# Kernel optimization log

Hardware: AMD Instinct MI355X
Metric: run time of the kernel (lower is better)

Reference implementation:

```python
import jax, jax.numpy as jnp
import numpy as np

KH = KW = 3
K = KH * KW
PAD = 1


def conv3x3(x, w, b):
    # x: [B,C,H,W], w: [O,C,3,3], b: [O]
    y = jax.lax.conv_general_dilated(x, w, (1, 1), ((PAD, PAD), (PAD, PAD)),
                                     dimension_numbers=('NCHW', 'OIHW', 'NCHW'))
    return y + b[None, :, None, None]


def deform_conv(x, offsets, w, b):
    # torchvision DeformConv2d, stride=1, pad=1, dilation=1, groups=1, offset_groups=1
    # x: [B,C,H,W], offsets: [B,2*K,H,W] ordered (dy,dx) per kernel point, w: [O,C,3,3]
    B, C, H, W = x.shape
    O = w.shape[0]
    off = offsets.reshape(B, K, 2, H, W)
    dy, dx = off[:, :, 0], off[:, :, 1]                      # [B,K,H,W]
    kyy, kxx = jnp.meshgrid(jnp.arange(KH), jnp.arange(KW), indexing='ij')
    ky = kyy.reshape(K).astype(x.dtype)
    kx = kxx.reshape(K).astype(x.dtype)
    py = dy + ky[None, :, None, None] + jnp.arange(H, dtype=x.dtype)[None, None, :, None] - PAD
    px = dx + kx[None, :, None, None] + jnp.arange(W, dtype=x.dtype)[None, None, None, :] - PAD
    y0 = jnp.floor(py)
    x0 = jnp.floor(px)
    wy = (py - y0)[:, None]                                   # [B,1,K,H,W]
    wx = (px - x0)[:, None]
    y0i = y0.astype(jnp.int32)
    x0i = x0.astype(jnp.int32)
    xf = x.reshape(B, C, H * W)

    def gather(yi, xi):
        valid = (yi >= 0) & (yi < H) & (xi >= 0) & (xi < W)   # zero outside
        yc = jnp.clip(yi, 0, H - 1)
        xc = jnp.clip(xi, 0, W - 1)
        idx = (yc * W + xc).reshape(B, 1, K * H * W)
        g = jnp.take_along_axis(xf, idx, axis=2).reshape(B, C, K, H, W)
        return g * valid[:, None].astype(x.dtype)

    v00 = gather(y0i, x0i)
    v01 = gather(y0i, x0i + 1)
    v10 = gather(y0i + 1, x0i)
    v11 = gather(y0i + 1, x0i + 1)
    samp = (v00 * (1 - wy) * (1 - wx) + v01 * (1 - wy) * wx
            + v10 * wy * (1 - wx) + v11 * wy * wx)            # [B,C,K,H,W]
    out = jnp.einsum('bckhw,ock->bohw', samp, w.reshape(O, C, K))
    return out + b[None, :, None, None]


def deform_align(x, y, wo, bo, wd, bd):
    return deform_conv(x, conv3x3(y, wo, bo), wd, bd)


def setup_inputs() -> dict:
    key = jax.random.key(0)
    ks = jax.random.split(key, 16)
    inC, embedC = 64, 96
    B, H, W = 4, 96, 96
    s = 0.02
    d = {
        'x1': jax.random.normal(ks[0], (B, inC, H, W), jnp.float32),
        'y': jax.random.normal(ks[1], (B, inC, H, W), jnp.float32),
        # block 1: offset conv inC->2K, deform conv inC->embedC
        'wo1': jax.random.normal(ks[2], (2 * K, inC, 3, 3), jnp.float32) * s,
        'bo1': jnp.zeros((2 * K,), jnp.float32),
        'wd1': jax.random.normal(ks[3], (embedC, inC, 3, 3), jnp.float32) * s,
        'bd1': jnp.zeros((embedC,), jnp.float32),
        # block 2: embedC->2K, embedC->embedC
        'wo2': jax.random.normal(ks[4], (2 * K, embedC, 3, 3), jnp.float32) * s,
        'bo2': jnp.zeros((2 * K,), jnp.float32),
        'wd2': jax.random.normal(ks[5], (embedC, embedC, 3, 3), jnp.float32) * s,
        'bd2': jnp.zeros((embedC,), jnp.float32),
        # block 3: embedC->2K, embedC->inC
        'wo3': jax.random.normal(ks[6], (2 * K, embedC, 3, 3), jnp.float32) * s,
        'bo3': jnp.zeros((2 * K,), jnp.float32),
        'wd3': jax.random.normal(ks[7], (inC, embedC, 3, 3), jnp.float32) * s,
        'bd3': jnp.zeros((inC,), jnp.float32),
    }
    return d


def reference(x1, y, wo1, bo1, wd1, bd1, wo2, bo2, wd2, bd2, wo3, bo3, wd3, bd3):
    h = deform_align(x1, y, wo1, bo1, wd1, bd1)
    h = deform_align(h, h, wo2, bo2, wd2, bd2)
    h = deform_align(h, h, wo3, bo3, wd3, bd3)
    return h
```

## Files before the change

kernel.cpp:

```cpp
#include <hip/hip_runtime.h>

constexpr int B = 4, H = 96, W = 96, HW = H * W;
constexpr int NPIX = B * HW;
constexpr int KOFF = 18;

typedef _Float16 half8 __attribute__((ext_vector_type(8)));
typedef _Float16 half4 __attribute__((ext_vector_type(4)));
typedef float f32x4 __attribute__((ext_vector_type(4)));
typedef __attribute__((address_space(3))) _Float16 lf16;

__device__ __forceinline__ int iclamp(int v, int lo, int hi) {
  return v < lo ? lo : (v > hi ? hi : v);
}

struct Corners {
  int i00, i01, i10, i11;
  float w00, w01, w10, w11;
};

__device__ __forceinline__ Corners mk_corners(float py, float qx) {
  float fy = floorf(py), fx = floorf(qx);
  float wy = py - fy, wx = qx - fx;
  int y0 = (int)fy, x0 = (int)fx;
  int y1 = y0 + 1, x1 = x0 + 1;
  bool vy0 = (y0 >= 0) & (y0 < H);
  bool vy1 = (y1 >= 0) & (y1 < H);
  bool vx0 = (x0 >= 0) & (x0 < W);
  bool vx1 = (x1 >= 0) & (x1 < W);
  int r0 = iclamp(y0, 0, H - 1) * W;
  int r1 = iclamp(y1, 0, H - 1) * W;
  int c0 = iclamp(x0, 0, W - 1);
  int c1 = iclamp(x1, 0, W - 1);
  Corners cc;
  cc.i00 = r0 + c0; cc.i01 = r0 + c1; cc.i10 = r1 + c0; cc.i11 = r1 + c1;
  float a = 1.f - wy, bb = 1.f - wx;
  cc.w00 = a * bb * ((vy0 & vx0) ? 1.f : 0.f);
  cc.w01 = a * wx * ((vy0 & vx1) ? 1.f : 0.f);
  cc.w10 = wy * bb * ((vy1 & vx0) ? 1.f : 0.f);
  cc.w11 = wy * wx * ((vy1 & vx1) ? 1.f : 0.f);
  return cc;
}

__device__ __forceinline__ void vm_wait0() {
  asm volatile("s_waitcnt vmcnt(0)" ::: "memory");
  __builtin_amdgcn_sched_barrier(0);
}

__device__ __forceinline__ void gld_lds16(const _Float16* g, lf16* l) {
  __builtin_amdgcn_global_load_lds(
      (const __attribute__((address_space(1))) void*)g,
      (__attribute__((address_space(3))) void*)l, 16, 0, 0);
}

template <int NF>
__device__ __forceinline__ void stage_frags(const _Float16* wk, lf16* lb, int lane) {
#pragma unroll
  for (int f = 0; f < NF; ++f)
    gld_lds16(wk + (size_t)f * 512 + lane * 8, lb + f * 512);
}

template <int KS>
__device__ __forceinline__ void load_corners(const _Float16* xb, int ch, const Corners& cc,
                                             half8 r[KS][4]) {
  const _Float16* p00 = xb + (size_t)cc.i00 * (KS * 32) + ch;
  const _Float16* p01 = xb + (size_t)cc.i01 * (KS * 32) + ch;
  const _Float16* p10 = xb + (size_t)cc.i10 * (KS * 32) + ch;
  const _Float16* p11 = xb + (size_t)cc.i11 * (KS * 32) + ch;
#pragma unroll
  for (int ks = 0; ks < KS; ++ks) {
    r[ks][0] = *(const half8*)(p00 + ks * 32);
    r[ks][1] = *(const half8*)(p01 + ks * 32);
    r[ks][2] = *(const half8*)(p10 + ks * 32);
    r[ks][3] = *(const half8*)(p11 + ks * 32);
  }
}

template <int KS>
__device__ __forceinline__ void interp_corners(const Corners& cc, half8 r[KS][4],
                                               half8 a[KS]) {
  _Float16 q00 = (_Float16)cc.w00, q01 = (_Float16)cc.w01;
  _Float16 q10 = (_Float16)cc.w10, q11 = (_Float16)cc.w11;
#pragma unroll
  for (int ks = 0; ks < KS; ++ks)
    a[ks] = r[ks][0] * q00 + r[ks][1] * q01 + r[ks][2] * q10 + r[ks][3] * q11;
}

template <int KS>
__device__ __forceinline__ void load_shift(const _Float16* xb, int ch, int h, int w,
                                           int ky, int kx, half8 a[KS]) {
  int yy = h + ky, xx = w + kx;
  bool v = (yy >= 0) & (yy < H) & (xx >= 0) & (xx < W);
  int yc = iclamp(yy, 0, H - 1), xc = iclamp(xx, 0, W - 1);
  const _Float16* pv = xb + (size_t)(yc * W + xc) * (KS * 32) + ch;
#pragma unroll
  for (int ks = 0; ks < KS; ++ks) {
    half8 r = *(const half8*)(pv + ks * 32);
    half8 z = {0, 0, 0, 0, 0, 0, 0, 0};
    a[ks] = v ? r : z;
  }
}

template <int KS, int NJ>
__device__ __forceinline__ void mfma_lds(const _Float16* lb, int lane,
                                         half8 a[KS], f32x4 acc[NJ]) {
#pragma unroll
  for (int ks = 0; ks < KS; ++ks)
#pragma unroll
    for (int j = 0; j < NJ; ++j) {
      half8 b = *(const half8*)(lb + (ks * NJ + j) * 512 + lane * 8);
      acc[j] = __builtin_amdgcn_mfma_f32_16x16x32_f16(a[ks], b, acc[j], 0, 0, 0);
    }
}

struct WAll {
  const float* src[6];
  _Float16* dst[6];
  int C[6], Osrc[6], OPAD[6], base[6];
};

__global__ void wfrag_all_kernel(WAll wa) {
  int bid = blockIdx.x;
  int s = 0;
#pragma unroll
  for (int i = 1; i < 6; ++i) s += (bid >= wa.base[i]) ? 1 : 0;
  int fid = bid - wa.base[s];
  int C = wa.C[s], Osrc = wa.Osrc[s], OPAD = wa.OPAD[s];
  const float* wsrc = wa.src[s];
  _Float16* wf = wa.dst[s];
  int KS = C / 32;
  int NJ = OPAD / 16;
  int lane = threadIdx.x;
  int j = fid % NJ;
  int ks = (fid / NJ) % KS;
  int k = fid / (NJ * KS);
  int o = j * 16 + (lane & 15);
  int c0 = ks * 32 + (lane >> 4) * 8;
  half8 v;
#pragma unroll
  for (int u = 0; u < 8; ++u)
    v[u] = (o < Osrc) ? (_Float16)wsrc[((size_t)o * C + c0 + u) * 9 + k] : (_Float16)0.f;
  *(half8*)(wf + ((size_t)fid * 64 + lane) * 8) = v;
}

__global__ __launch_bounds__(256) void repack2_kernel(const float* __restrict__ in0,
                                                      const float* __restrict__ in1,
                                                      _Float16* __restrict__ o0,
                                                      _Float16* __restrict__ o1) {
  constexpr int C = 64;
  const float* in = blockIdx.y ? in1 : in0;
  _Float16* outh = blockIdx.y ? o1 : o0;
  __shared__ float tile[64 * C];
  int t = threadIdx.x;
  int pix0 = blockIdx.x * 64;
  int b = pix0 / HW;
  int hw0 = pix0 - b * HW;
  int l = t & 63;
  for (int cc = t >> 6; cc < C; cc += 4)
    tile[cc * 64 + l] = in[((size_t)b * C + cc) * HW + hw0 + l];
  __syncthreads();
  int pl = t >> 2;
  int cq = t & 3;
  _Float16* op = outh + (size_t)(pix0 + pl) * C + cq * (C / 4);
#pragma unroll
  for (int c = 0; c < C / 4; c += 4) {
    half4 hv;
#pragma unroll
    for (int u = 0; u < 4; ++u) hv[u] = (_Float16)tile[(cq * (C / 4) + c + u) * 64 + pl];
    *(half4*)(op + c) = hv;
  }
}

template <int C, int O, bool WF32, bool WH>
__global__ __launch_bounds__(64, 1)
void stage_kernel(const _Float16* __restrict__ xoff, const _Float16* __restrict__ xdef,
                  const _Float16* __restrict__ wfo, const float* __restrict__ bo,
                  const _Float16* __restrict__ wfd, const float* __restrict__ bd,
                  float* __restrict__ out, _Float16* __restrict__ outh) {
  constexpr int KS = C / 32;
  constexpr int NJ = O / 16;
  constexpr int NFD = KS * NJ;
  constexpr int NFO = KS * 2;
  __shared__ _Float16 ldsB[2 * NFD * 512];
  __shared__ float lofs[16][KOFF];
  lf16* lb3 = (lf16*)ldsB;
  const int lane = threadIdx.x;
  const int row = lane & 15;
  const int kgrp = lane >> 4;
  const int ch = kgrp * 8;
  const int chunk = (blockIdx.x & 7) * (int)(gridDim.x >> 3) + (blockIdx.x >> 3);
  const int px0 = chunk * 16;
  const int b = px0 / HW;
  const int hw0 = px0 - b * HW;
  const int hwm = hw0 + row;
  const int h0 = hwm / W, w0 = hwm - h0 * W;
  const _Float16* xo = xoff + (size_t)b * HW * C;
  const _Float16* xd = xdef + (size_t)b * HW * C;

  {
    f32x4 aoc[2];
#pragma unroll
    for (int j = 0; j < 2; ++j) {
      int o = j * 16 + row;
      float bv = (o < KOFF) ? bo[o] : 0.f;
      aoc[j] = {bv, bv, bv, bv};
    }
    half8 a[KS], n[KS];
    stage_frags<NFO>(wfo, lb3, lane);
    load_shift<KS>(xo, ch, h0, w0, -1, -1, a);
#pragma unroll
    for (int k = 0; k < 9; ++k) {
      vm_wait0();
      if (k < 8) {
        int kn = k + 1;
        stage_frags<NFO>(wfo + (size_t)kn * (NFO * 512),
                         lb3 + (kn & 1) * NFO * 512, lane);
        load_shift<KS>(xo, ch, h0, w0, kn / 3 - 1, kn % 3 - 1, n);
        __builtin_amdgcn_sched_barrier(0);
      }
      mfma_lds<KS, 2>(ldsB + (k & 1) * NFO * 512, lane, a, aoc);
      if (k < 8) {
#pragma unroll
        for (int ks = 0; ks < KS; ++ks) a[ks] = n[ks];
      }
    }
#pragma unroll
    for (int j = 0; j < 2; ++j) {
      int o = j * 16 + row;
      if (o < KOFF) {
#pragma unroll
        for (int r = 0; r < 4; ++r) lofs[kgrp * 4 + r][o] = aoc[j][r];
      }
    }
  }

  const float hf = (float)(h0 - 1), wwf = (float)(w0 - 1);

  f32x4 acc[NJ];
#pragma unroll
  for (int j = 0; j < NJ; ++j) {
    float bv = bd[j * 16 + row];
    acc[j] = {bv, bv, bv, bv};
  }
  half8 a[KS];
  half8 r[KS][4], rn[KS][4];
  Corners ccur = mk_corners(lofs[row][0] + hf, lofs[row][1] + wwf);
  stage_frags<NFD>(wfd, lb3 + NFD * 512, lane);
  load_corners<KS>(xd, ch, ccur, r);
#pragma unroll
  for (int k = 0; k < 9; ++k) {
    vm_wait0();
    if (k < 8) {
      int kn = k + 1;
      Corners cn = mk_corners(lofs[row][2 * kn] + hf + (float)(kn / 3),
                              lofs[row][2 * kn + 1] + wwf + (float)(kn % 3));
      stage_frags<NFD>(wfd + (size_t)kn * (NFD * 512),
                       lb3 + ((kn + 1) & 1) * NFD * 512, lane);
      load_corners<KS>(xd, ch, cn, rn);
      __builtin_amdgcn_sched_barrier(0);
      interp_corners<KS>(ccur, r, a);
      mfma_lds<KS, NJ>(ldsB + ((k + 1) & 1) * NFD * 512, lane, a, acc);
      ccur = cn;
#pragma unroll
      for (int ks = 0; ks < KS; ++ks)
#pragma unroll
        for (int q = 0; q < 4; ++q) r[ks][q] = rn[ks][q];
    } else {
      interp_corners<KS>(ccur, r, a);
      mfma_lds<KS, NJ>(ldsB + ((k + 1) & 1) * NFD * 512, lane, a, acc);
    }
  }
#pragma unroll
  for (int j = 0; j < NJ; ++j) {
    int o = j * 16 + row;
#pragma unroll
    for (int r2 = 0; r2 < 4; ++r2) {
      int p = px0 + kgrp * 4 + r2;
      if (WF32) out[((size_t)b * O + o) * HW + (p - b * HW)] = acc[j][r2];
      if (WH) outh[(size_t)p * O + o] = (_Float16)acc[j][r2];
    }
  }
}

extern "C" void kernel_launch(void* const* d_in, const int* in_sizes, int n_in,
                              void* d_out, int out_size, void* d_ws, size_t ws_size,
                              hipStream_t stream) {
  const float* x1  = (const float*)d_in[0];
  const float* y   = (const float*)d_in[1];
  const float* wo1 = (const float*)d_in[2];
  const float* bo1 = (const float*)d_in[3];
  const float* wd1 = (const float*)d_in[4];
  const float* bd1 = (const float*)d_in[5];
  const float* wo2 = (const float*)d_in[6];
  const float* bo2 = (const float*)d_in[7];
  const float* wd2 = (const float*)d_in[8];
  const float* bd2 = (const float*)d_in[9];
  const float* wo3 = (const float*)d_in[10];
  const float* bo3 = (const float*)d_in[11];
  const float* wd3 = (const float*)d_in[12];
  const float* bd3 = (const float*)d_in[13];
  float* out = (float*)d_out;

  char* p = (char*)d_ws;
  auto alloc = [&](size_t bytes) {
    char* r = p;
    p += (bytes + 255) & ~(size_t)255;
    return r;
  };
  _Float16* Wo1f = (_Float16*)alloc((size_t)9 * 2 * 2 * 512 * 2);
  _Float16* Wo2f = (_Float16*)alloc((size_t)9 * 3 * 2 * 512 * 2);
  _Float16* Wo3f = (_Float16*)alloc((size_t)9 * 3 * 2 * 512 * 2);
  _Float16* W1f  = (_Float16*)alloc((size_t)9 * 2 * 6 * 512 * 2);
  _Float16* W2f  = (_Float16*)alloc((size_t)9 * 3 * 6 * 512 * 2);
  _Float16* W3f  = (_Float16*)alloc((size_t)9 * 3 * 4 * 512 * 2);
  _Float16* x1h = (_Float16*)alloc((size_t)NPIX * 64 * 2);
  _Float16* yh  = (_Float16*)alloc((size_t)NPIX * 64 * 2);
  _Float16* h1h = (_Float16*)alloc((size_t)NPIX * 96 * 2);
  _Float16* h2h = (_Float16*)alloc((size_t)NPIX * 96 * 2);

  WAll wa;
  wa.src[0] = wo1; wa.dst[0] = Wo1f; wa.C[0] = 64; wa.Osrc[0] = 18; wa.OPAD[0] = 32;
  wa.src[1] = wo2; wa.dst[1] = Wo2f; wa.C[1] = 96; wa.Osrc[1] = 18; wa.OPAD[1] = 32;
  wa.src[2] = wo3; wa.dst[2] = Wo3f; wa.C[2] = 96; wa.Osrc[2] = 18; wa.OPAD[2] = 32;
  wa.src[3] = wd1; wa.dst[3] = W1f;  wa.C[3] = 64; wa.Osrc[3] = 96; wa.OPAD[3] = 96;
  wa.src[4] = wd2; wa.dst[4] = W2f;  wa.C[4] = 96; wa.Osrc[4] = 96; wa.OPAD[4] = 96;
  wa.src[5] = wd3; wa.dst[5] = W3f;  wa.C[5] = 96; wa.Osrc[5] = 64; wa.OPAD[5] = 64;
  int base = 0;
  for (int i = 0; i < 6; ++i) {
    wa.base[i] = base;
    base += 9 * (wa.C[i] / 32) * (wa.OPAD[i] / 16);
  }
  hipLaunchKernelGGL(wfrag_all_kernel, dim3(base), dim3(64), 0, stream, wa);
  hipLaunchKernelGGL(repack2_kernel, dim3(NPIX / 64, 2), dim3(256), 0, stream,
                     x1, y, x1h, yh);

  dim3 gs(NPIX / 16);
  dim3 wb(64);

  hipLaunchKernelGGL((stage_kernel<64, 96, false, true>), gs, wb, 0, stream,
                     yh, x1h, Wo1f, bo1, W1f, bd1, (float*)nullptr, h1h);
  hipLaunchKernelGGL((stage_kernel<96, 96, false, true>), gs, wb, 0, stream,
                     h1h, h1h, Wo2f, bo2, W2f, bd2, (float*)nullptr, h2h);
  hipLaunchKernelGGL((stage_kernel<96, 64, true, false>), gs, wb, 0, stream,
                     h2h, h2h, Wo3f, bo3, W3f, bd3, out, (_Float16*)nullptr);
}
```

Before: 135.5 us.

## Share LDS-staged weight fragments across four waves per block

Each block now holds four wavefronts covering 64 pixels instead of one wavefront covering 16. The weight fragments for each kernel tap are staged into LDS cooperatively, with each wave loading a quarter, and all four waves then read the shared double-buffered copy. Per-wave vmcnt waits are replaced by block-wide __syncthreads. This cuts redundant weight staging and raises the number of resident waves per CU for the same LDS footprint, at the cost of coupling the four waves through a barrier on every tap.

```diff
diff --git a/kernel.cpp b/kernel.cpp
--- a/kernel.cpp
+++ b/kernel.cpp
@@ -41,11 +41,6 @@
   return cc;
 }
 
-__device__ __forceinline__ void vm_wait0() {
-  asm volatile("s_waitcnt vmcnt(0)" ::: "memory");
-  __builtin_amdgcn_sched_barrier(0);
-}
-
 __device__ __forceinline__ void gld_lds16(const _Float16* g, lf16* l) {
   __builtin_amdgcn_global_load_lds(
       (const __attribute__((address_space(1))) void*)g,
@@ -53,10 +48,14 @@
 }
 
 template <int NF>
-__device__ __forceinline__ void stage_frags(const _Float16* wk, lf16* lb, int lane) {
-#pragma unroll
-  for (int f = 0; f < NF; ++f)
-    gld_lds16(wk + (size_t)f * 512 + lane * 8, lb + f * 512);
+__device__ __forceinline__ void stage_coop(const _Float16* wk, lf16* lb, int lane,
+                                           int wid) {
+#pragma unroll
+  for (int i = 0; i < (NF + 3) / 4; ++i) {
+    int f = i * 4 + wid;
+    if (f < NF)
+      gld_lds16(wk + (size_t)f * 512 + lane * 8, lb + f * 512);
+  }
 }
 
 template <int KS>
@@ -171,7 +170,7 @@
 }
 
 template <int C, int O, bool WF32, bool WH>
-__global__ __launch_bounds__(64, 1)
+__global__ __launch_bounds__(256, 1)
 void stage_kernel(const _Float16* __restrict__ xoff, const _Float16* __restrict__ xdef,
                   const _Float16* __restrict__ wfo, const float* __restrict__ bo,
                   const _Float16* __restrict__ wfd, const float* __restrict__ bd,
@@ -181,14 +180,16 @@
   constexpr int NFD = KS * NJ;
   constexpr int NFO = KS * 2;
   __shared__ _Float16 ldsB[2 * NFD * 512];
-  __shared__ float lofs[16][KOFF];
+  __shared__ float lofs[64][KOFF];
   lf16* lb3 = (lf16*)ldsB;
-  const int lane = threadIdx.x;
+  const int tid = threadIdx.x;
+  const int wid = tid >> 6;
+  const int lane = tid & 63;
   const int row = lane & 15;
   const int kgrp = lane >> 4;
   const int ch = kgrp * 8;
   const int chunk = (blockIdx.x & 7) * (int)(gridDim.x >> 3) + (blockIdx.x >> 3);
-  const int px0 = chunk * 16;
+  const int px0 = chunk * 64 + wid * 16;
   const int b = px0 / HW;
   const int hw0 = px0 - b * HW;
   const int hwm = hw0 + row;
@@ -205,19 +206,18 @@
       aoc[j] = {bv, bv, bv, bv};
     }
     half8 a[KS], n[KS];
-    stage_frags<NFO>(wfo, lb3, lane);
+    stage_coop<NFO>(wfo, lb3, lane, wid);
     load_shift<KS>(xo, ch, h0, w0, -1, -1, a);
 #pragma unroll
     for (int k = 0; k < 9; ++k) {
-      vm_wait0();
+      __syncthreads();
       if (k < 8) {
         int kn = k + 1;
-        stage_frags<NFO>(wfo + (size_t)kn * (NFO * 512),
-                         lb3 + (kn & 1) * NFO * 512, lane);
+        stage_coop<NFO>(wfo + (size_t)kn * (NFO * 512),
+                        lb3 + (kn & 1) * NFD * 512, lane, wid);
         load_shift<KS>(xo, ch, h0, w0, kn / 3 - 1, kn % 3 - 1, n);
-        __builtin_amdgcn_sched_barrier(0);
       }
-      mfma_lds<KS, 2>(ldsB + (k & 1) * NFO * 512, lane, a, aoc);
+      mfma_lds<KS, 2>(ldsB + (k & 1) * NFD * 512, lane, a, aoc);
       if (k < 8) {
 #pragma unroll
         for (int ks = 0; ks < KS; ++ks) a[ks] = n[ks];
@@ -228,11 +228,13 @@
       int o = j * 16 + row;
       if (o < KOFF) {
 #pragma unroll
-        for (int r = 0; r < 4; ++r) lofs[kgrp * 4 + r][o] = aoc[j][r];
+        for (int r = 0; r < 4; ++r) lofs[wid * 16 + kgrp * 4 + r][o] = aoc[j][r];
       }
     }
   }
-
+  __syncthreads();
+
+  const int prow = wid * 16 + row;
   const float hf = (float)(h0 - 1), wwf = (float)(w0 - 1);
 
   f32x4 acc[NJ];
@@ -243,22 +245,21 @@
   }
   half8 a[KS];
   half8 r[KS][4], rn[KS][4];
-  Corners ccur = mk_corners(lofs[row][0] + hf, lofs[row][1] + wwf);
-  stage_frags<NFD>(wfd, lb3 + NFD * 512, lane);
+  Corners ccur = mk_corners(lofs[prow][0] + hf, lofs[prow][1] + wwf);
+  stage_coop<NFD>(wfd, lb3, lane, wid);
   load_corners<KS>(xd, ch, ccur, r);
 #pragma unroll
   for (int k = 0; k < 9; ++k) {
-    vm_wait0();
+    __syncthreads();
     if (k < 8) {
       int kn = k + 1;
-      Corners cn = mk_corners(lofs[row][2 * kn] + hf + (float)(kn / 3),
-                              lofs[row][2 * kn + 1] + wwf + (float)(kn % 3));
-      stage_frags<NFD>(wfd + (size_t)kn * (NFD * 512),
-                       lb3 + ((kn + 1) & 1) * NFD * 512, lane);
+      stage_coop<NFD>(wfd + (size_t)kn * (NFD * 512),
+                      lb3 + (kn & 1) * NFD * 512, lane, wid);
+      Corners cn = mk_corners(lofs[prow][2 * kn] + hf + (float)(kn / 3),
+                              lofs[prow][2 * kn + 1] + wwf + (float)(kn % 3));
       load_corners<KS>(xd, ch, cn, rn);
-      __builtin_amdgcn_sched_barrier(0);
       interp_corners<KS>(ccur, r, a);
-      mfma_lds<KS, NJ>(ldsB + ((k + 1) & 1) * NFD * 512, lane, a, acc);
+      mfma_lds<KS, NJ>(ldsB + (k & 1) * NFD * 512, lane, a, acc);
       ccur = cn;
 #pragma unroll
       for (int ks = 0; ks < KS; ++ks)
@@ -266,7 +267,7 @@
         for (int q = 0; q < 4; ++q) r[ks][q] = rn[ks][q];
     } else {
       interp_corners<KS>(ccur, r, a);
-      mfma_lds<KS, NJ>(ldsB + ((k + 1) & 1) * NFD * 512, lane, a, acc);
+      mfma_lds<KS, NJ>(ldsB + (k & 1) * NFD * 512, lane, a, acc);
     }
   }
 #pragma unroll
@@ -333,8 +334,8 @@
   hipLaunchKernelGGL(repack2_kernel, dim3(NPIX / 64, 2), dim3(256), 0, stream,
                      x1, y, x1h, yh);
 
-  dim3 gs(NPIX / 16);
-  dim3 wb(64);
+  dim3 gs(NPIX / 64);
+  dim3 wb(256);
 
   hipLaunchKernelGGL((stage_kernel<64, 96, false, true>), gs, wb, 0, stream,
                      yh, x1h, Wo1f, bo1, W1f, bd1, (float*)nullptr, h1h);
```

Result: faster. 121.4 us (-10.4%).
